# Optimization experiments

Hardware: AMD Instinct MI355X
Metric: run time of the kernel (lower is better)

Reference implementation:

```python
import jax, jax.numpy as jnp
import numpy as np

B, H, W, C = 32, 56, 56, 256
NH, WS, SHIFT = 8, 7, 3
S = WS * WS            # tokens per window = 49
CH = C // NH           # channels per head = 32
EPS = 1e-5


def layer_norm(x, w, b):
    mu = jnp.mean(x, axis=-1, keepdims=True)
    var = jnp.var(x, axis=-1, keepdims=True)
    return (x - mu) * jax.lax.rsqrt(var + EPS) * w + b


def spatial_mlp(x, weight, bias):
    # x: (B, H*W, C); weight: (NH*S, S, 1) grouped-conv1d weight; bias: (NH*S,)
    xr = x.reshape(B, H, W, C)
    if SHIFT > 0:
        P_l, P_r, P_t, P_b = WS - SHIFT, SHIFT, WS - SHIFT, SHIFT
        xr = jnp.pad(xr, ((0, 0), (P_t, P_b), (P_l, P_r), (0, 0)))
    Hp, Wp = xr.shape[1], xr.shape[2]
    # window partition -> (nW, S, NH, CH)
    win = xr.reshape(B, Hp // WS, WS, Wp // WS, WS, C)
    win = win.transpose(0, 1, 3, 2, 4, 5).reshape(-1, S, NH, CH)
    # grouped 1x1 conv == per-head token-mixing matrix (S x S)
    wgt = weight.reshape(NH, S, S)             # wgt[h, i, j]
    out = jnp.einsum('hij,njhd->nihd', wgt, win)
    out = out + bias.reshape(NH, S).T[None, :, :, None]
    # window reverse -> (B, Hp, Wp, C)
    out = out.reshape(B, Hp // WS, Wp // WS, WS, WS, C)
    out = out.transpose(0, 1, 3, 2, 4, 5).reshape(B, Hp, Wp, C)
    if SHIFT > 0:
        out = out[:, P_t:Hp - P_b, P_l:Wp - P_r, :]
    return out.reshape(B, H * W, C)


def mlp(x, fc1_w, fc1_b, fc2_w, fc2_b):
    h = jax.nn.gelu(x @ fc1_w + fc1_b, approximate=False)
    return h @ fc2_w + fc2_b


def setup_inputs() -> dict:
    key = jax.random.key(0)
    ks = jax.random.split(key, 5)
    sc = 0.02
    return {
        'x': jax.random.normal(ks[0], (B, H * W, C), jnp.float32),
        'norm1_w': jnp.ones((C,), jnp.float32),
        'norm1_b': jnp.zeros((C,), jnp.float32),
        'spatial_w': jax.random.normal(ks[1], (NH * S, S, 1), jnp.float32) * sc,
        'spatial_b': jax.random.normal(ks[2], (NH * S,), jnp.float32) * sc,
        'norm2_w': jnp.ones((C,), jnp.float32),
        'norm2_b': jnp.zeros((C,), jnp.float32),
        'fc1_w': jax.random.normal(ks[3], (C, 4 * C), jnp.float32) * sc,
        'fc1_b': jnp.zeros((4 * C,), jnp.float32),
        'fc2_w': jax.random.normal(ks[4], (4 * C, C), jnp.float32) * sc,
        'fc2_b': jnp.zeros((C,), jnp.float32),
    }


def reference(x, norm1_w, norm1_b, spatial_w, spatial_b, norm2_w, norm2_b,
              fc1_w, fc1_b, fc2_w, fc2_b):
    shortcut = x
    h = layer_norm(x, norm1_w, norm1_b)
    h = spatial_mlp(h, spatial_w, spatial_b)
    x = shortcut + h                      # drop_path = 0 (eval)
    x = x + mlp(layer_norm(x, norm2_w, norm2_b), fc1_w, fc1_b, fc2_w, fc2_b)
    return x
```

## Files before the change

kernel.cpp:

```cpp
#include <hip/hip_runtime.h>
#include <hip/hip_bf16.h>

#define NHEAD 8
#define IMG   3136
#define MTOT  100352
#define NWIN  1296

typedef __attribute__((ext_vector_type(2))) _Float16 f16x2;
typedef __attribute__((ext_vector_type(4))) float    f32x4;
typedef __attribute__((ext_vector_type(16))) float   f32x16;
typedef __attribute__((ext_vector_type(8))) short    bf16x8;
typedef __attribute__((ext_vector_type(2))) int      i32x2;
typedef __attribute__((ext_vector_type(4))) int      i32x4;

#define SWZA(byteoff, r) ((byteoff) ^ (((r)&7)<<4) ^ ((((r)>>3)&1)<<7))

__device__ __forceinline__ short f2bf(float f){
  union { float fv; unsigned u; } a; a.fv = f;
  unsigned u = a.u;
  unsigned r = (u + 0x7fffu + ((u >> 16) & 1u)) >> 16;
  return (short)r;
}

__device__ __forceinline__ unsigned cvtpk(float lo, float hi){
  unsigned r;
  asm("v_cvt_pk_bf16_f32 %0, %1, %2" : "=v"(r) : "v"(lo), "v"(hi));
  return r;
}

__device__ __forceinline__ float gelu_s(float v){
  float e = __expf(-1.702f*v);
  return v*__builtin_amdgcn_rcpf(1.f + e);
}

__global__ void prep_k(const float* __restrict__ spw, short* __restrict__ wspA)
{
  int t = threadIdx.x;
  #pragma unroll
  for (int k = 0; k < 16; ++k) {
    int idx = t + k*256;
    int lane = idx & 63;
    int kt = (idx >> 6) & 3;
    int mt = (idx >> 8) & 1;
    int h  = idx >> 9;
    int i  = mt*32 + (lane & 31);
    int jb = kt*16 + (lane >> 5)*8;
    bf16x8 o;
    #pragma unroll
    for (int e = 0; e < 8; ++e) {
      int j = jb + e;
      float v = (i < 49 && j < 49) ? spw[(size_t)(h*49 + i)*49 + j] : 0.f;
      o[e] = f2bf(v);
    }
    *(bf16x8*)(wspA + (size_t)idx*8) = o;
  }
}

__global__ __launch_bounds__(512,4) void win_k(
    const float* __restrict__ x, const float* __restrict__ n1w, const float* __restrict__ n1b,
    const float* __restrict__ spb, const short* __restrict__ wspA,
    float* __restrict__ x1,
    const float* __restrict__ fc1w, const float* __restrict__ fc2w,
    short* __restrict__ w1p, short* __restrict__ w2p)
{
  int bid = blockIdx.x;
  int t = threadIdx.x;

  if (bid >= NWIN) {
    int fb = bid - NWIN;
    if (fb < 64) {
      int id = fb*512 + t;
      int l = id & 63, fk = id >> 6;
      int kk = fk & 15, f = fk >> 4;
      int n = f*32 + (l & 31);
      int kbase = kk*16 + (l >> 5)*8;
      bf16x8 o;
      #pragma unroll
      for (int e = 0; e < 8; ++e) o[e] = f2bf(fc1w[(size_t)(kbase+e)*1024 + n]);
      *(bf16x8*)(w1p + (size_t)id*8) = o;
    } else {
      int id = (fb-64)*512 + t;
      int l = id & 63, fk = id >> 6;
      int kk = fk & 63, f = fk >> 6;
      int n = f*32 + (l & 31);
      int kbase = kk*16 + (l >> 5)*8;
      bf16x8 o;
      #pragma unroll
      for (int e = 0; e < 8; ++e) o[e] = f2bf(fc2w[(size_t)(kbase+e)*256 + n]);
      *(bf16x8*)(w2p + (size_t)id*8) = o;
    }
    return;
  }

  extern __shared__ char wsm[];
  char*  lxT  = wsm;
  float* murs = (float*)(wsm + 65536);
  int lane = t & 63, wave = t >> 6;

  {
    f32x4 xv[2][7];
    #pragma unroll
    for (int w = 0; w < 2; ++w) {
      int win = bid*2 + w;
      int b = win/81, rem = win - b*81, wi = rem/9, wj = rem - (rem/9)*9;
      #pragma unroll
      for (int j = 0; j < 7; ++j) {
        int i = wave + 8*j;
        int iy = i/7, ix = i - iy*7;
        int hh = wi*7 + iy - 4, ww = wj*7 + ix - 4;
        bool valid = (i < 49) && hh >= 0 && hh < 56 && ww >= 0 && ww < 56;
        if (valid)
          xv[w][j] = *(const f32x4*)(x + ((size_t)(b*IMG + hh*56 + ww))*256 + lane*4);
      }
    }
    #pragma unroll
    for (int w = 0; w < 2; ++w) {
      int win = bid*2 + w;
      int b = win/81, rem = win - b*81, wi = rem/9, wj = rem - (rem/9)*9;
      #pragma unroll
      for (int j = 0; j < 7; ++j) {
        int i = wave + 8*j;
        int iy = i/7, ix = i - iy*7;
        int hh = wi*7 + iy - 4, ww = wj*7 + ix - 4;
        bool valid = (i < 49) && hh >= 0 && hh < 56 && ww >= 0 && ww < 56;
        if (!valid) continue;
        f32x4 v = xv[w][j];
        float s  = v[0]+v[1]+v[2]+v[3];
        float s2 = v[0]*v[0]+v[1]*v[1]+v[2]*v[2]+v[3]*v[3];
        #pragma unroll
        for (int m = 1; m < 64; m <<= 1) { s += __shfl_xor(s, m); s2 += __shfl_xor(s2, m); }
        float mu = s * (1.f/256.f);
        float rs = rsqrtf(s2*(1.f/256.f) - mu*mu + 1e-5f);
        if (lane == 0) { murs[(w*56+i)*2] = mu; murs[(w*56+i)*2+1] = rs; }
      }
    }
  }
  __syncthreads();

  {
    int w = t >> 8, c = t & 255;
    int win = bid*2 + w;
    int b = win/81, rem = win - b*81, wi = rem/9, wj = rem - (rem/9)*9;
    float nwc = n1w[c], nbc = n1b[c];
    char* rowb = lxT + c*256;
    #pragma unroll
    for (int cj = 0; cj < 7; ++cj) {
      float vals[8];
      #pragma unroll
      for (int e = 0; e < 8; ++e) {
        int p = cj*8 + e;
        float fv = 0.f;
        if (p < 49) {
          int iy = p/7, ix = p - iy*7;
          int hh = wi*7 + iy - 4, ww = wj*7 + ix - 4;
          if (hh >= 0 && hh < 56 && ww >= 0 && ww < 56) {
            float mu = murs[(w*56+p)*2], rs = murs[(w*56+p)*2+1];
            float xv = x[((size_t)(b*IMG + hh*56 + ww))*256 + c];
            fv = (xv - mu)*rs*nwc + nbc;
          }
        }
        vals[e] = fv;
      }
      i32x4 pk;
      pk[0] = cvtpk(vals[0], vals[1]); pk[1] = cvtpk(vals[2], vals[3]);
      pk[2] = cvtpk(vals[4], vals[5]); pk[3] = cvtpk(vals[6], vals[7]);
      *(i32x4*)(rowb + SWZA(w*128 + cj*16, c)) = pk;
    }
    i32x4 z = {0,0,0,0};
    *(i32x4*)(rowb + SWZA(w*128 + 112, c)) = z;
  }
  __syncthreads();

  int h = wave, d = lane & 31, lk = lane >> 5;
  const short* wA = wspA + h*4096;
  int c = h*32 + d;
  f32x16 a00, a01, a10, a11;
  #pragma unroll
  for (int q = 0; q < 16; ++q) { a00[q]=0.f; a01[q]=0.f; a10[q]=0.f; a11[q]=0.f; }
  #pragma unroll
  for (int kt = 0; kt < 4; ++kt) {
    bf16x8 A0 = *(const bf16x8*)(wA + (kt*64 + lane)*8);
    bf16x8 A1 = *(const bf16x8*)(wA + ((4+kt)*64 + lane)*8);
    int bo = kt*32 + lk*16;
    bf16x8 B0 = *(const bf16x8*)(lxT + c*256 + SWZA(bo, c));
    bf16x8 B1 = *(const bf16x8*)(lxT + c*256 + SWZA(128 + bo, c));
    a00 = __builtin_amdgcn_mfma_f32_32x32x16_bf16(A0, B0, a00, 0,0,0);
    a10 = __builtin_amdgcn_mfma_f32_32x32x16_bf16(A1, B0, a10, 0,0,0);
    a01 = __builtin_amdgcn_mfma_f32_32x32x16_bf16(A0, B1, a01, 0,0,0);
    a11 = __builtin_amdgcn_mfma_f32_32x32x16_bf16(A1, B1, a11, 0,0,0);
  }

  #pragma unroll
  for (int w = 0; w < 2; ++w) {
    int win = bid*2 + w;
    int b = win/81, rem = win - b*81, wi = rem/9, wj = rem - (rem/9)*9;
    #pragma unroll
    for (int mt = 0; mt < 2; ++mt) {
      #pragma unroll
      for (int r = 0; r < 16; ++r) {
        int i = mt*32 + (r&3) + 8*(r>>2) + 4*lk;
        if (i < 49) {
          int iy = i/7, ix = i - iy*7;
          int hh = wi*7 + iy - 4, ww = wj*7 + ix - 4;
          if (hh >= 0 && hh < 56 && ww >= 0 && ww < 56) {
            size_t off = ((size_t)(b*IMG + hh*56 + ww))*256 + c;
            float av = mt==0 ? (w==0 ? a00[r] : a01[r]) : (w==0 ? a10[r] : a11[r]);
            x1[off] = x[off] + av + spb[h*49 + i];
          }
        }
      }
    }
  }
}

__global__ __launch_bounds__(512,4) void mlp_k(
    const float* __restrict__ x1, float* __restrict__ out,
    const short* __restrict__ w1p, const short* __restrict__ w2p,
    const float* __restrict__ n2w, const float* __restrict__ n2b,
    const float* __restrict__ b1, const float* __restrict__ b2)
{
  extern __shared__ char sm[];
  char* a2  = sm;
  char* hcb = sm + 32768;

  int t = threadIdx.x, lane = t & 63, wave = t >> 6;
  int m0 = blockIdx.x * 64;

  {
    f32x4 nw = *(const f32x4*)(n2w + lane*4);
    f32x4 nb = *(const f32x4*)(n2b + lane*4);
    #pragma unroll
    for (int rq = 0; rq < 8; ++rq) {
      int rr = wave*8 + rq;
      f32x4 v = *(const f32x4*)(x1 + (size_t)(m0+rr)*256 + lane*4);
      float s  = v[0]+v[1]+v[2]+v[3];
      float s2 = v[0]*v[0]+v[1]*v[1]+v[2]*v[2]+v[3]*v[3];
      #pragma unroll
      for (int m = 1; m < 64; m <<= 1){ s += __shfl_xor(s,m); s2 += __shfl_xor(s2,m); }
      float mu = s*(1.f/256.f);
      float rs = rsqrtf(s2*(1.f/256.f) - mu*mu + 1e-5f);
      float y0 = (v[0]-mu)*rs*nw[0] + nb[0];
      float y1 = (v[1]-mu)*rs*nw[1] + nb[1];
      float y2 = (v[2]-mu)*rs*nw[2] + nb[2];
      float y3 = (v[3]-mu)*rs*nw[3] + nb[3];
      i32x2 pk; pk[0] = cvtpk(y0,y1); pk[1] = cvtpk(y2,y3);
      *(i32x2*)(a2 + SWZA(lane*8, rr) + rr*512) = pk;
    }
  }
  __syncthreads();

  int lr = lane & 31, lk = lane >> 5;
  int wn = wave;

  f32x16 accO[2];
  #pragma unroll
  for (int i=0;i<2;++i)
    #pragma unroll
    for (int q=0;q<16;++q) accO[i][q] = 0.f;

  for (int ch = 0; ch < 4; ++ch) {
    f32x16 accH[2];
    #pragma unroll
    for (int i=0;i<2;++i)
      #pragma unroll
      for (int q=0;q<16;++q) accH[i][q] = 0.f;

    const short* w1f = w1p + ((size_t)((ch*8 + wn)*16)*64 + lane)*8;
    bf16x8 bq[4];
    #pragma unroll
    for (int k = 0; k < 4; ++k) bq[k] = *(const bf16x8*)(w1f + (size_t)k*512);
    __builtin_amdgcn_s_setprio(1);
    #pragma unroll
    for (int kk = 0; kk < 16; ++kk) {
      bf16x8 b = bq[kk & 3];
      if (kk < 12) bq[kk & 3] = *(const bf16x8*)(w1f + (size_t)(kk+4)*512);
      int kb = kk*32 + lk*16;
      bf16x8 a0 = *(const bf16x8*)(a2 + SWZA(kb, lr) + lr*512);
      bf16x8 a1 = *(const bf16x8*)(a2 + SWZA(kb, 32+lr) + (32+lr)*512);
      accH[0] = __builtin_amdgcn_mfma_f32_32x32x16_bf16(a0, b, accH[0], 0,0,0);
      accH[1] = __builtin_amdgcn_mfma_f32_32x32x16_bf16(a1, b, accH[1], 0,0,0);
    }
    __builtin_amdgcn_s_setprio(0);

    {
      float b1v = b1[ch*256 + wn*32 + lr];
      int colb = (wn*32 + lr)*2;
      #pragma unroll
      for (int ms = 0; ms < 2; ++ms) {
        #pragma unroll
        for (int r2 = 0; r2 < 8; ++r2) {
          int r = r2*2;
          float g0 = gelu_s(accH[ms][r]   + b1v);
          float g1 = gelu_s(accH[ms][r+1] + b1v);
          unsigned pw = cvtpk(g0, g1);
          int row0 = ms*32 + (r&3) + 8*(r>>2) + 4*lk;
          int row1 = row0 + 1;
          *(short*)(hcb + SWZA(colb, row0) + row0*512) = (short)(pw & 0xffffu);
          *(short*)(hcb + SWZA(colb, row1) + row1*512) = (short)(pw >> 16);
        }
      }
    }
    __syncthreads();

    const short* w2f = w2p + ((size_t)(wn*64 + ch*16)*64 + lane)*8;
    #pragma unroll
    for (int k = 0; k < 4; ++k) bq[k] = *(const bf16x8*)(w2f + (size_t)k*512);
    __builtin_amdgcn_s_setprio(1);
    #pragma unroll
    for (int kk = 0; kk < 16; ++kk) {
      bf16x8 b = bq[kk & 3];
      if (kk < 12) bq[kk & 3] = *(const bf16x8*)(w2f + (size_t)(kk+4)*512);
      int kb = kk*32 + lk*16;
      bf16x8 a0 = *(const bf16x8*)(hcb + SWZA(kb, lr) + lr*512);
      bf16x8 a1 = *(const bf16x8*)(hcb + SWZA(kb, 32+lr) + (32+lr)*512);
      accO[0] = __builtin_amdgcn_mfma_f32_32x32x16_bf16(a0, b, accO[0], 0,0,0);
      accO[1] = __builtin_amdgcn_mfma_f32_32x32x16_bf16(a1, b, accO[1], 0,0,0);
    }
    __builtin_amdgcn_s_setprio(0);
    if (ch < 3) __syncthreads();
  }

  {
    int col = wn*32 + lr;
    float b2v = b2[col];
    #pragma unroll
    for (int ms = 0; ms < 2; ++ms) {
      #pragma unroll
      for (int r = 0; r < 16; ++r) {
        int row = ms*32 + (r&3) + 8*(r>>2) + 4*lk;
        size_t off = (size_t)(m0 + row)*256 + col;
        out[off] = x1[off] + accO[ms][r] + b2v;
      }
    }
  }
}

extern "C" void kernel_launch(void* const* d_in, const int* in_sizes, int n_in,
                              void* d_out, int out_size, void* d_ws, size_t ws_size,
                              hipStream_t stream) {
  const float* x    = (const float*)d_in[0];
  const float* n1w  = (const float*)d_in[1];
  const float* n1b  = (const float*)d_in[2];
  const float* spw  = (const float*)d_in[3];
  const float* spb  = (const float*)d_in[4];
  const float* n2w  = (const float*)d_in[5];
  const float* n2b  = (const float*)d_in[6];
  const float* fc1w = (const float*)d_in[7];
  const float* fc1b = (const float*)d_in[8];
  const float* fc2w = (const float*)d_in[9];
  const float* fc2b = (const float*)d_in[10];
  float* outp = (float*)d_out;

  char* ws = (char*)d_ws;
  short* w1p  = (short*)ws;
  short* w2p  = (short*)(ws + 524288);
  short* wspA = (short*)(ws + 1048576);

  prep_k<<<1, 256, 0, stream>>>(spw, wspA);

  hipFuncSetAttribute(reinterpret_cast<const void*>(win_k),
                      hipFuncAttributeMaxDynamicSharedMemorySize, 66432);
  win_k<<<NWIN + 128, 512, 66432, stream>>>(x, n1w, n1b, spb, wspA, outp,
                                            fc1w, fc2w, w1p, w2p);

  hipFuncSetAttribute(reinterpret_cast<const void*>(mlp_k),
                      hipFuncAttributeMaxDynamicSharedMemorySize, 65536);
  mlp_k<<<MTOT/64, 512, 65536, stream>>>(outp, outp, w1p, w2p, n2w, n2b, fc1b, fc2b);
}
```

Baseline: 288.2 us.

## Retile MLP kernel waves as 2x4 grid with smaller hidden chunks and LDS

Reorganizes the eight waves of the fused MLP kernel from eight column slices into a 2x4 grid of row and column tiles. The hidden dimension is now processed in eight chunks of 128 instead of four chunks of 256, which halves the hidden-activation LDS buffer and cuts dynamic shared memory from 64 KiB to 48 KiB. In the second GEMM each wave reuses one A fragment across two B fragments, lowering LDS reads per MFMA. The trade-off is twice as many chunk iterations and block barriers, plus a different weight-fetch pattern.

```diff
diff --git a/kernel.cpp b/kernel.cpp
--- a/kernel.cpp
+++ b/kernel.cpp
@@ -14,6 +14,7 @@
 typedef __attribute__((ext_vector_type(4))) int      i32x4;
 
 #define SWZA(byteoff, r) ((byteoff) ^ (((r)&7)<<4) ^ ((((r)>>3)&1)<<7))
+#define SWZC(byteoff, r) ((byteoff) ^ (((r)&7)<<4) ^ ((((r)>>3)&1)<<7))
 
 __device__ __forceinline__ short f2bf(float f){
   union { float fv; unsigned u; } a; a.fv = f;
@@ -250,7 +251,10 @@
   __syncthreads();
 
   int lr = lane & 31, lk = lane >> 5;
-  int wn = wave;
+  int wm = wave >> 2, wn = wave & 3;
+  int arow = wm*32 + lr;
+  char* a2r = a2 + arow*512;
+  char* hcr = hcb + arow*256;
 
   f32x16 accO[2];
   #pragma unroll
@@ -258,14 +262,12 @@
     #pragma unroll
     for (int q=0;q<16;++q) accO[i][q] = 0.f;
 
-  for (int ch = 0; ch < 4; ++ch) {
-    f32x16 accH[2];
-    #pragma unroll
-    for (int i=0;i<2;++i)
-      #pragma unroll
-      for (int q=0;q<16;++q) accH[i][q] = 0.f;
-
-    const short* w1f = w1p + ((size_t)((ch*8 + wn)*16)*64 + lane)*8;
+  for (int ch = 0; ch < 8; ++ch) {
+    f32x16 accH;
+    #pragma unroll
+    for (int q=0;q<16;++q) accH[q] = 0.f;
+
+    const short* w1f = w1p + ((size_t)((ch*4 + wn)*16)*64 + lane)*8;
     bf16x8 bq[4];
     #pragma unroll
     for (int k = 0; k < 4; ++k) bq[k] = *(const bf16x8*)(w1f + (size_t)k*512);
@@ -275,62 +277,62 @@
       bf16x8 b = bq[kk & 3];
       if (kk < 12) bq[kk & 3] = *(const bf16x8*)(w1f + (size_t)(kk+4)*512);
       int kb = kk*32 + lk*16;
-      bf16x8 a0 = *(const bf16x8*)(a2 + SWZA(kb, lr) + lr*512);
-      bf16x8 a1 = *(const bf16x8*)(a2 + SWZA(kb, 32+lr) + (32+lr)*512);
-      accH[0] = __builtin_amdgcn_mfma_f32_32x32x16_bf16(a0, b, accH[0], 0,0,0);
-      accH[1] = __builtin_amdgcn_mfma_f32_32x32x16_bf16(a1, b, accH[1], 0,0,0);
+      bf16x8 a0 = *(const bf16x8*)(a2r + SWZA(kb, arow));
+      accH = __builtin_amdgcn_mfma_f32_32x32x16_bf16(a0, b, accH, 0,0,0);
     }
     __builtin_amdgcn_s_setprio(0);
 
     {
-      float b1v = b1[ch*256 + wn*32 + lr];
+      float b1v = b1[ch*128 + wn*32 + lr];
       int colb = (wn*32 + lr)*2;
       #pragma unroll
-      for (int ms = 0; ms < 2; ++ms) {
-        #pragma unroll
-        for (int r2 = 0; r2 < 8; ++r2) {
-          int r = r2*2;
-          float g0 = gelu_s(accH[ms][r]   + b1v);
-          float g1 = gelu_s(accH[ms][r+1] + b1v);
-          unsigned pw = cvtpk(g0, g1);
-          int row0 = ms*32 + (r&3) + 8*(r>>2) + 4*lk;
-          int row1 = row0 + 1;
-          *(short*)(hcb + SWZA(colb, row0) + row0*512) = (short)(pw & 0xffffu);
-          *(short*)(hcb + SWZA(colb, row1) + row1*512) = (short)(pw >> 16);
-        }
+      for (int r2 = 0; r2 < 8; ++r2) {
+        int r = r2*2;
+        float g0 = gelu_s(accH[r]   + b1v);
+        float g1v = gelu_s(accH[r+1] + b1v);
+        unsigned pw = cvtpk(g0, g1v);
+        int row0 = wm*32 + (r&3) + 8*(r>>2) + 4*lk;
+        int row1 = row0 + 1;
+        *(short*)(hcb + SWZC(colb, row0) + row0*256) = (short)(pw & 0xffffu);
+        *(short*)(hcb + SWZC(colb, row1) + row1*256) = (short)(pw >> 16);
       }
     }
     __syncthreads();
 
-    const short* w2f = w2p + ((size_t)(wn*64 + ch*16)*64 + lane)*8;
-    #pragma unroll
-    for (int k = 0; k < 4; ++k) bq[k] = *(const bf16x8*)(w2f + (size_t)k*512);
+    const short* w2f = w2p + ((size_t)((wn*2)*64 + ch*8)*64 + lane)*8;
+    bq[0] = *(const bf16x8*)(w2f + (size_t)0);
+    bq[1] = *(const bf16x8*)(w2f + (size_t)32768);
+    bq[2] = *(const bf16x8*)(w2f + (size_t)512);
+    bq[3] = *(const bf16x8*)(w2f + (size_t)32768 + 512);
     __builtin_amdgcn_s_setprio(1);
     #pragma unroll
-    for (int kk = 0; kk < 16; ++kk) {
-      bf16x8 b = bq[kk & 3];
-      if (kk < 12) bq[kk & 3] = *(const bf16x8*)(w2f + (size_t)(kk+4)*512);
+    for (int kk = 0; kk < 8; ++kk) {
+      bf16x8 b0, b1f;
+      if ((kk&1)==0) { b0 = bq[0]; b1f = bq[1]; } else { b0 = bq[2]; b1f = bq[3]; }
+      if (kk < 6) {
+        bf16x8 n0 = *(const bf16x8*)(w2f + (size_t)(kk+2)*512);
+        bf16x8 n1 = *(const bf16x8*)(w2f + (size_t)32768 + (size_t)(kk+2)*512);
+        if ((kk&1)==0) { bq[0] = n0; bq[1] = n1; } else { bq[2] = n0; bq[3] = n1; }
+      }
       int kb = kk*32 + lk*16;
-      bf16x8 a0 = *(const bf16x8*)(hcb + SWZA(kb, lr) + lr*512);
-      bf16x8 a1 = *(const bf16x8*)(hcb + SWZA(kb, 32+lr) + (32+lr)*512);
-      accO[0] = __builtin_amdgcn_mfma_f32_32x32x16_bf16(a0, b, accO[0], 0,0,0);
-      accO[1] = __builtin_amdgcn_mfma_f32_32x32x16_bf16(a1, b, accO[1], 0,0,0);
+      bf16x8 a0 = *(const bf16x8*)(hcr + SWZC(kb, arow));
+      accO[0] = __builtin_amdgcn_mfma_f32_32x32x16_bf16(a0, b0, accO[0], 0,0,0);
+      accO[1] = __builtin_amdgcn_mfma_f32_32x32x16_bf16(a0, b1f, accO[1], 0,0,0);
     }
     __builtin_amdgcn_s_setprio(0);
-    if (ch < 3) __syncthreads();
-  }
-
-  {
-    int col = wn*32 + lr;
+    if (ch < 7) __syncthreads();
+  }
+
+  #pragma unroll
+  for (int ns = 0; ns < 2; ++ns) {
+    int col = wn*64 + ns*32 + lr;
     float b2v = b2[col];
     #pragma unroll
-    for (int ms = 0; ms < 2; ++ms) {
-      #pragma unroll
-      for (int r = 0; r < 16; ++r) {
-        int row = ms*32 + (r&3) + 8*(r>>2) + 4*lk;
-        size_t off = (size_t)(m0 + row)*256 + col;
-        out[off] = x1[off] + accO[ms][r] + b2v;
-      }
+    for (int r = 0; r < 16; ++r) {
+      int row = wm*32 + (r&3) + 8*(r>>2) + 4*lk;
+      size_t off = (size_t)(m0 + row)*256 + col;
+      float av = ns==0 ? accO[0][r] : accO[1][r];
+      out[off] = x1[off] + av + b2v;
     }
   }
 }
@@ -364,6 +366,6 @@
                                             fc1w, fc2w, w1p, w2p);
 
   hipFuncSetAttribute(reinterpret_cast<const void*>(mlp_k),
-                      hipFuncAttributeMaxDynamicSharedMemorySize, 65536);
-  mlp_k<<<MTOT/64, 512, 65536, stream>>>(outp, outp, w1p, w2p, n2w, n2b, fc1b, fc2b);
-}
+                      hipFuncAttributeMaxDynamicSharedMemorySize, 49152);
+  mlp_k<<<MTOT/64, 512, 49152, stream>>>(outp, outp, w1p, w2p, n2w, n2b, fc1b, fc2b);
+}
```

After: 320.0 us. 11.0% more time.
